# Optimization experiments

Measured on AMD Instinct MI355X. Metric: run time of the kernel, lower is better.

Reference implementation:

```python
import jax, jax.numpy as jnp
import numpy as np
from jax import lax

BATCH = 4096
SEQ = 200
VOCAB = 100000
HID = 128


def setup_inputs() -> dict:
    key = jax.random.key(0)
    k0, k1, k2, k3, k4 = jax.random.split(key, 5)
    inputs = jax.random.randint(k0, (BATCH, SEQ), 0, VOCAB, dtype=jnp.int32).astype(jnp.int64)
    emb = jax.random.normal(k1, (VOCAB, HID), dtype=jnp.float32) * 0.05
    # Keras GRU (reset_after=True): kernel [H,3H], recurrent_kernel [H,3H], bias [2,3H]
    kernel = jax.random.normal(k2, (HID, 3 * HID), dtype=jnp.float32) * (1.0 / np.sqrt(HID))
    rec_kernel = jax.random.normal(k3, (HID, 3 * HID), dtype=jnp.float32) * (1.0 / np.sqrt(HID))
    bias = jax.random.normal(k4, (2, 3 * HID), dtype=jnp.float32) * 0.01
    return {"inputs": inputs, "emb": emb, "kernel": kernel, "rec_kernel": rec_kernel, "bias": bias}


def _masked_gru(x, mask, kernel, rec_kernel, bias):
    # x: [B,S,H] embedded inputs; mask: [B,S] bool (True = valid timestep)
    input_bias, rec_bias = bias[0], bias[1]
    # Precompute all input projections in one big GEMM: [B,S,3H]
    xproj = jnp.einsum('bsh,hk->bsk', x, kernel) + input_bias
    B, H = x.shape[0], x.shape[2]

    def step(h, scan_in):
        xp, m = scan_in  # xp: [B,3H], m: [B]
        hp = h @ rec_kernel + rec_bias  # [B,3H]
        xz, xr, xh = xp[:, :H], xp[:, H:2 * H], xp[:, 2 * H:]
        hz, hr, hh_rec = hp[:, :H], hp[:, H:2 * H], hp[:, 2 * H:]
        z = jax.nn.sigmoid(xz + hz)
        r = jax.nn.sigmoid(xr + hr)
        hh = jnp.tanh(xh + r * hh_rec)  # reset_after=True: r applied after recurrent matmul
        h_new = z * h + (1.0 - z) * hh
        # mask_zero semantics: masked steps carry previous state through
        h_new = jnp.where(m[:, None], h_new, h)
        return h_new, None

    h0 = jnp.zeros((B, H), dtype=x.dtype)
    xs = (jnp.swapaxes(xproj, 0, 1), jnp.swapaxes(mask, 0, 1))  # time-major
    h_final, _ = lax.scan(step, h0, xs)
    return h_final  # [B,H] == last valid-step output under Keras masking


def reference(inputs, emb, kernel, rec_kernel, bias):
    x = emb[inputs]              # [B,S,H] embedding lookup
    mask = inputs != 0           # mask_zero=True
    return _masked_gru(x, mask, kernel, rec_kernel, bias)
```

## Files before the change

### kernel.cpp

```cpp
#include <hip/hip_runtime.h>

#define BATCH 4096
#define SEQ   200
#define HID   128
#define ROWS  16
#define NTH   512
#define XPAD  136

typedef _Float16 f16;
typedef f16 f16x4 __attribute__((ext_vector_type(4)));
typedef f16 f16x8 __attribute__((ext_vector_type(8)));
typedef float f32x4 __attribute__((ext_vector_type(4)));

#define MFMA(a, b, c) __builtin_amdgcn_mfma_f32_16x16x32_f16((a), (b), (c), 0, 0, 0)

__device__ __forceinline__ float fast_exp2(float x) {
#if defined(__has_builtin) && __has_builtin(__builtin_amdgcn_exp2f)
    return __builtin_amdgcn_exp2f(x);
#else
    float r; asm volatile("v_exp_f32 %0, %1\n\ts_nop 0" : "=v"(r) : "v"(x)); return r;
#endif
}
__device__ __forceinline__ float fast_rcp(float x) {
#if defined(__has_builtin) && __has_builtin(__builtin_amdgcn_rcpf)
    return __builtin_amdgcn_rcpf(x);
#else
    float r; asm volatile("v_rcp_f32 %0, %1\n\ts_nop 0" : "=v"(r) : "v"(x)); return r;
#endif
}
#define LOG2E  1.442695041f
#define LOG2E2 2.885390082f

__global__ __attribute__((amdgpu_flat_work_group_size(NTH, NTH)))
void gru_mfma(const int* __restrict__ inputs,
              const float* __restrict__ emb,
              const float* __restrict__ kernel,
              const float* __restrict__ rec_kernel,
              const float* __restrict__ bias,
              float* __restrict__ out)
{
    __shared__ __align__(16) f16 Wt[HID][XPAD];
    __shared__ __align__(16) f16 x16[2][ROWS][XPAD];
    __shared__ __align__(16) f16 h16[2][ROWS][XPAD];
    __shared__ int tok_sh[2][ROWS];
    __shared__ int ts_sh;

    const int tid  = threadIdx.x;
    const int lane = tid & 63;
    const int j0   = (tid >> 6) * 16;
    const int l15  = lane & 15;
    const int hi   = lane >> 4;
    const int r0   = hi * 4;
    const int row0 = blockIdx.x * ROWS;

    if (tid == 0) { int any = 0; for (int i = 1; i < 128; i += 2) any |= inputs[i]; ts_sh = any ? 1 : 2; }

    for (int i = tid; i < HID * HID; i += NTH) {
        const int c = i & 127, k = i >> 7;
        Wt[c][k] = (f16)rec_kernel[(size_t)k * 384 + 256 + c];
    }

    f16x8 Bx[3][4];
    f16x8 Brz[4], Brr[4];
#pragma unroll
    for (int g = 0; g < 3; ++g)
#pragma unroll
        for (int kt = 0; kt < 4; ++kt) {
            f16x8 t;
#pragma unroll
            for (int e = 0; e < 8; ++e)
                t[e] = (f16)kernel[(size_t)(kt * 32 + hi * 8 + e) * 384 + g * HID + j0 + l15];
            Bx[g][kt] = t;
        }
#pragma unroll
    for (int kt = 0; kt < 4; ++kt) {
        f16x8 tz, tr;
#pragma unroll
        for (int e = 0; e < 8; ++e) {
            const size_t krow = (size_t)(kt * 32 + hi * 8 + e) * 384;
            tz[e] = (f16)rec_kernel[krow + j0 + l15];
            tr[e] = (f16)rec_kernel[krow + HID + j0 + l15];
        }
        Brz[kt] = tz; Brr[kt] = tr;
    }

    const float bz  = bias[j0 + l15]       + bias[384 + j0 + l15];
    const float br  = bias[128 + j0 + l15] + bias[512 + j0 + l15];
    const float bxh = bias[256 + j0 + l15];
    const float brh = bias[640 + j0 + l15];

    f32x4 h = {0.f, 0.f, 0.f, 0.f};

    __syncthreads();
    const int ts = ts_sh;

    const int rr = tid >> 5;
    const int c4 = (tid & 31) * 4;

    {
        const int tok0 = inputs[((size_t)(row0 + rr) * SEQ + 0) * ts];
        if ((tid & 31) == 0) tok_sh[0][rr] = tok0;
        const float4 ev = *(const float4*)&emb[(size_t)tok0 * HID + c4];
        f16x4 xv; xv[0] = (f16)ev.x; xv[1] = (f16)ev.y; xv[2] = (f16)ev.z; xv[3] = (f16)ev.w;
        *(f16x4*)&x16[0][rr][c4] = xv;
        for (int i = tid; i < ROWS * XPAD; i += NTH) ((f16*)h16[0])[i] = (f16)0.f;
    }
    int tokA = inputs[((size_t)(row0 + rr) * SEQ + 1) * ts];
    __syncthreads();

    for (int s = 0; s < SEQ; ++s) {
        const int cur = s & 1, nxt = cur ^ 1;
        const bool pf = (s + 1 < SEQ);
        float4 ev; int tokB = tokA;
        if (pf) {
            ev = *(const float4*)&emb[(size_t)tokA * HID + c4];
            const int s2 = (s + 2 < SEQ) ? (s + 2) : (SEQ - 1);
            tokB = inputs[((size_t)(row0 + rr) * SEQ + s2) * ts];
        }

        f32x4 az = {bz, bz, bz, bz}, ar = {br, br, br, br};
        f32x4 ax = {bxh, bxh, bxh, bxh}, ah = {brh, brh, brh, brh};
#pragma unroll
        for (int kt = 0; kt < 4; ++kt) {
            const int ko = kt * 32 + hi * 8;
            const f16x8 xa = *(const f16x8*)&x16[cur][l15][ko];
            const f16x8 ha = *(const f16x8*)&h16[cur][l15][ko];
            az = MFMA(xa, Bx[0][kt], az);
            ar = MFMA(xa, Bx[1][kt], ar);
            ax = MFMA(xa, Bx[2][kt], ax);
            az = MFMA(ha, Brz[kt], az);
            ar = MFMA(ha, Brr[kt], ar);
            const f16x8 rh = *(const f16x8*)&Wt[j0 + l15][ko];
            ah = MFMA(ha, rh, ah);
        }

#pragma unroll
        for (int i = 0; i < 4; ++i) {
            const int tk = tok_sh[cur][r0 + i];
            const float z  = fast_rcp(1.f + fast_exp2(-LOG2E  * az[i]));
            const float rg = fast_rcp(1.f + fast_exp2(-LOG2E  * ar[i]));
            const float u  = ax[i] + rg * ah[i];
            const float hh = 1.f - 2.f * fast_rcp(1.f + fast_exp2(LOG2E2 * u));
            const float hn = z * h[i] + (1.f - z) * hh;
            h[i] = (tk != 0) ? hn : h[i];
        }

#pragma unroll
        for (int i = 0; i < 4; ++i) h16[nxt][r0 + i][j0 + l15] = (f16)h[i];
        if (pf) {
            f16x4 xv; xv[0] = (f16)ev.x; xv[1] = (f16)ev.y; xv[2] = (f16)ev.z; xv[3] = (f16)ev.w;
            *(f16x4*)&x16[nxt][rr][c4] = xv;
            if ((tid & 31) == 0) tok_sh[nxt][rr] = tokA;
            tokA = tokB;
        }
        __syncthreads();
    }

#pragma unroll
    for (int i = 0; i < 4; ++i)
        out[(size_t)(row0 + r0 + i) * HID + j0 + l15] = h[i];
}

extern "C" void kernel_launch(void* const* d_in, const int* in_sizes, int n_in,
                              void* d_out, int out_size, void* d_ws, size_t ws_size,
                              hipStream_t stream) {
    const int* inputs      = (const int*)d_in[0];
    const float* emb       = (const float*)d_in[1];
    const float* kernel    = (const float*)d_in[2];
    const float* rec_k     = (const float*)d_in[3];
    const float* bias      = (const float*)d_in[4];
    float* out             = (float*)d_out;
    gru_mfma<<<BATCH / ROWS, NTH, 0, stream>>>(inputs, emb, kernel, rec_k, bias, out);
}
```

Baseline: 192.9 us.

## Store LDS operands in MFMA fragment order and fold activation scales into weights

Shared-memory copies of x, h and the recurrent candidate weights are stored in the exact per-lane fragment order the 16x16x32 MFMA reads, so each lane loads 16 contiguous bytes without padding or strided address arithmetic. The -log2e and 2*log2e activation scale factors are folded into the fp16 weights and biases, which removes the per-element multiplies before exp2 on the serial recurrence path. The state update is also rewritten as a single fused form. Scaling the weights before fp16 rounding slightly changes numerics, and the h scatter writes now use a different bank pattern.

```diff
diff --git a/kernel.cpp b/kernel.cpp
--- a/kernel.cpp
+++ b/kernel.cpp
@@ -5,7 +5,6 @@
 #define HID   128
 #define ROWS  16
 #define NTH   512
-#define XPAD  136
 
 typedef _Float16 f16;
 typedef f16 f16x4 __attribute__((ext_vector_type(4)));
@@ -39,15 +38,16 @@
               const float* __restrict__ bias,
               float* __restrict__ out)
 {
-    __shared__ __align__(16) f16 Wt[HID][XPAD];
-    __shared__ __align__(16) f16 x16[2][ROWS][XPAD];
-    __shared__ __align__(16) f16 h16[2][ROWS][XPAD];
+    __shared__ __align__(16) f16 Wtf[8][4][64][8];
+    __shared__ __align__(16) f16 xf[2][4][64][8];
+    __shared__ __align__(16) f16 hf[2][4][64][8];
     __shared__ int tok_sh[2][ROWS];
     __shared__ int ts_sh;
 
     const int tid  = threadIdx.x;
     const int lane = tid & 63;
-    const int j0   = (tid >> 6) * 16;
+    const int wv   = tid >> 6;
+    const int j0   = wv * 16;
     const int l15  = lane & 15;
     const int hi   = lane >> 4;
     const int r0   = hi * 4;
@@ -55,13 +55,16 @@
 
     if (tid == 0) { int any = 0; for (int i = 1; i < 128; i += 2) any |= inputs[i]; ts_sh = any ? 1 : 2; }
 
-    for (int i = tid; i < HID * HID; i += NTH) {
-        const int c = i & 127, k = i >> 7;
-        Wt[c][k] = (f16)rec_kernel[(size_t)k * 384 + 256 + c];
+    for (int i = tid; i < 8 * 4 * 64 * 8; i += NTH) {
+        const int e = i & 7, ln = (i >> 3) & 63, kt = (i >> 9) & 3, w = i >> 11;
+        const int c = w * 16 + (ln & 15);
+        const int k = kt * 32 + (ln >> 4) * 8 + e;
+        ((f16*)Wtf)[i] = (f16)(LOG2E2 * rec_kernel[(size_t)k * 384 + 256 + c]);
     }
 
     f16x8 Bx[3][4];
     f16x8 Brz[4], Brr[4];
+    const float gsc[3] = { -LOG2E, -LOG2E, LOG2E2 };
 #pragma unroll
     for (int g = 0; g < 3; ++g)
 #pragma unroll
@@ -69,7 +72,7 @@
             f16x8 t;
 #pragma unroll
             for (int e = 0; e < 8; ++e)
-                t[e] = (f16)kernel[(size_t)(kt * 32 + hi * 8 + e) * 384 + g * HID + j0 + l15];
+                t[e] = (f16)(gsc[g] * kernel[(size_t)(kt * 32 + hi * 8 + e) * 384 + g * HID + j0 + l15]);
             Bx[g][kt] = t;
         }
 #pragma unroll
@@ -78,32 +81,36 @@
 #pragma unroll
         for (int e = 0; e < 8; ++e) {
             const size_t krow = (size_t)(kt * 32 + hi * 8 + e) * 384;
-            tz[e] = (f16)rec_kernel[krow + j0 + l15];
-            tr[e] = (f16)rec_kernel[krow + HID + j0 + l15];
+            tz[e] = (f16)(-LOG2E * rec_kernel[krow + j0 + l15]);
+            tr[e] = (f16)(-LOG2E * rec_kernel[krow + HID + j0 + l15]);
         }
         Brz[kt] = tz; Brr[kt] = tr;
     }
 
-    const float bz  = bias[j0 + l15]       + bias[384 + j0 + l15];
-    const float br  = bias[128 + j0 + l15] + bias[512 + j0 + l15];
-    const float bxh = bias[256 + j0 + l15];
-    const float brh = bias[640 + j0 + l15];
+    const float bz  = -LOG2E * (bias[j0 + l15]       + bias[384 + j0 + l15]);
+    const float br  = -LOG2E * (bias[128 + j0 + l15] + bias[512 + j0 + l15]);
+    const float bxh =  LOG2E2 * bias[256 + j0 + l15];
+    const float brh =  LOG2E2 * bias[640 + j0 + l15];
 
     f32x4 h = {0.f, 0.f, 0.f, 0.f};
+
+    const int cw  = j0 + l15;
+    const int hwi = ((cw >> 5) * 64 + ((cw >> 3) & 3) * 16 + r0) * 8 + (cw & 7);
 
     __syncthreads();
     const int ts = ts_sh;
 
     const int rr = tid >> 5;
     const int c4 = (tid & 31) * 4;
+    const int xwi = ((c4 >> 5) * 64 + ((c4 >> 3) & 3) * 16 + rr) * 8 + (c4 & 7);
 
     {
         const int tok0 = inputs[((size_t)(row0 + rr) * SEQ + 0) * ts];
         if ((tid & 31) == 0) tok_sh[0][rr] = tok0;
         const float4 ev = *(const float4*)&emb[(size_t)tok0 * HID + c4];
         f16x4 xv; xv[0] = (f16)ev.x; xv[1] = (f16)ev.y; xv[2] = (f16)ev.z; xv[3] = (f16)ev.w;
-        *(f16x4*)&x16[0][rr][c4] = xv;
-        for (int i = tid; i < ROWS * XPAD; i += NTH) ((f16*)h16[0])[i] = (f16)0.f;
+        *(f16x4*)&((f16*)xf)[xwi] = xv;
+        for (int i = tid; i < 4 * 64 * 8; i += NTH) ((f16*)hf)[i] = (f16)0.f;
     }
     int tokA = inputs[((size_t)(row0 + rr) * SEQ + 1) * ts];
     __syncthreads();
@@ -122,34 +129,36 @@
         f32x4 ax = {bxh, bxh, bxh, bxh}, ah = {brh, brh, brh, brh};
 #pragma unroll
         for (int kt = 0; kt < 4; ++kt) {
-            const int ko = kt * 32 + hi * 8;
-            const f16x8 xa = *(const f16x8*)&x16[cur][l15][ko];
-            const f16x8 ha = *(const f16x8*)&h16[cur][l15][ko];
+            const f16x8 xa = *(const f16x8*)&xf[cur][kt][lane][0];
+            const f16x8 ha = *(const f16x8*)&hf[cur][kt][lane][0];
             az = MFMA(xa, Bx[0][kt], az);
             ar = MFMA(xa, Bx[1][kt], ar);
             ax = MFMA(xa, Bx[2][kt], ax);
             az = MFMA(ha, Brz[kt], az);
             ar = MFMA(ha, Brr[kt], ar);
-            const f16x8 rh = *(const f16x8*)&Wt[j0 + l15][ko];
+            const f16x8 rh = *(const f16x8*)&Wtf[wv][kt][lane][0];
             ah = MFMA(ha, rh, ah);
         }
 
 #pragma unroll
         for (int i = 0; i < 4; ++i) {
             const int tk = tok_sh[cur][r0 + i];
-            const float z  = fast_rcp(1.f + fast_exp2(-LOG2E  * az[i]));
-            const float rg = fast_rcp(1.f + fast_exp2(-LOG2E  * ar[i]));
+            const float z  = fast_rcp(1.f + fast_exp2(az[i]));
+            const float rg = fast_rcp(1.f + fast_exp2(ar[i]));
             const float u  = ax[i] + rg * ah[i];
-            const float hh = 1.f - 2.f * fast_rcp(1.f + fast_exp2(LOG2E2 * u));
-            const float hn = z * h[i] + (1.f - z) * hh;
+            const float hh = 1.f - 2.f * fast_rcp(1.f + fast_exp2(u));
+            const float hn = hh + z * (h[i] - hh);
             h[i] = (tk != 0) ? hn : h[i];
         }
 
+        {
+            f16* hp = &((f16*)hf)[nxt * 4 * 64 * 8 + hwi];
 #pragma unroll
-        for (int i = 0; i < 4; ++i) h16[nxt][r0 + i][j0 + l15] = (f16)h[i];
+            for (int i = 0; i < 4; ++i) hp[i * 8] = (f16)h[i];
+        }
         if (pf) {
             f16x4 xv; xv[0] = (f16)ev.x; xv[1] = (f16)ev.y; xv[2] = (f16)ev.z; xv[3] = (f16)ev.w;
-            *(f16x4*)&x16[nxt][rr][c4] = xv;
+            *(f16x4*)&((f16*)xf)[nxt * 4 * 64 * 8 + xwi] = xv;
             if ((tid & 31) == 0) tok_sh[nxt][rr] = tokA;
             tokA = tokB;
         }
```

Result: faster. 182.5 us (-5.4%).
